# Performance work log

Hardware: AMD Instinct MI355X
Metric: run time of the kernel (lower is better)

The kernel has to match this reference:

```python
import math
import jax, jax.numpy as jnp
import numpy as np

B, S, HIDDEN = 1, 4096, 2048
HEADS, KVH = 16, 4
HD = HIDDEN // HEADS            # 128
GROUPS = HEADS // KVH           # 4
CHUNK = 1024                    # ring_attention_chunk_size
BASE = 500000.0
MAXPOS = 131072
ORIG = 8192
BFAST, BSLOW, MSCALE_CFG = 32.0, 1.0, 1.0
SCALING = MAXPOS / ORIG


def _yarn_inv_freq():
    dim = HD
    pos_freqs = BASE ** (np.arange(0, dim, 2, dtype=np.float32) / dim)
    extrap = 1.0 / pos_freqs
    interp = 1.0 / (SCALING * pos_freqs)
    low = max(math.floor(dim * math.log(ORIG / (BFAST * 2 * math.pi)) / (2 * math.log(BASE))), 0)
    high = min(math.ceil(dim * math.log(ORIG / (BSLOW * 2 * math.pi)) / (2 * math.log(BASE))), dim - 1)
    i = np.arange(dim // 2, dtype=np.float32)
    smooth = np.clip((i - low) / max(high - low, 1), 0.0, 1.0)  # i<low -> interp, i>high -> extrap
    inv = (1.0 - smooth) * interp + smooth * extrap
    return jnp.asarray(inv, jnp.float32)

INV_FREQ = _yarn_inv_freq()
MSCALE = (0.1 * math.log(SCALING) + 1.0) * MSCALE_CFG  # scaling > 1


def rotate_half(x):
    x1, x2 = jnp.split(x, 2, axis=-1)
    return jnp.concatenate((-x2, x1), axis=-1)


def ring_attention(q, k, v, chunk, causal=True):
    # q,k,v: [B,H,S,D]; kv_len divisible by chunk
    b, h, s, d = q.shape
    kv_len = k.shape[2]
    nc = kv_len // chunk
    scale = d ** (-0.5)
    k_chunks = jnp.moveaxis(k.reshape(b, h, nc, chunk, d), 2, 0)  # [nc,B,H,chunk,D]
    v_chunks = jnp.moveaxis(v.reshape(b, h, nc, chunk, d), 2, 0)
    kv_starts = jnp.arange(nc) * chunk
    q_idx = jnp.arange(s)[:, None]
    k_off = jnp.arange(chunk)[None, :]
    neg_inf = jnp.float32(-jnp.inf)

    def step(carry, inp):
        out, mx, se = carry
        kch, vch, kv_start = inp
        scores = jnp.einsum('bhqd,bhkd->bhqk', q, kch) * scale
        if causal:
            mask = (kv_start + k_off) > q_idx  # [S, chunk]
            scores = jnp.where(mask[None, None], neg_inf, scores)
        chunk_max = scores.max(axis=-1, keepdims=True)
        new_max = jnp.maximum(mx, chunk_max)
        exp_old = se * jnp.exp(mx - new_max)
        exp_chunk = jnp.exp(scores - new_max)
        exp_sum_chunk = exp_chunk.sum(axis=-1, keepdims=True)
        denom = exp_old + exp_sum_chunk + 1e-10
        out = out * (se / denom) + jnp.einsum('bhqk,bhkd->bhqd', exp_chunk, vch) / denom
        return (out, new_max, exp_old + exp_sum_chunk), None

    init = (jnp.zeros_like(q),
            jnp.full((b, h, s, 1), -jnp.inf, dtype=q.dtype),
            jnp.zeros((b, h, s, 1), dtype=q.dtype))
    (out, _, _), _ = jax.lax.scan(step, init, (k_chunks, v_chunks, kv_starts))
    return out


def setup_inputs() -> dict:
    key = jax.random.key(0)
    ks = jax.random.split(key, 5)
    hidden_states = jax.random.normal(ks[0], (B, S, HIDDEN), dtype=jnp.float32)
    position_ids = jnp.broadcast_to(jnp.arange(S, dtype=jnp.int32)[None, :], (B, S))
    sd = 1.0 / math.sqrt(HIDDEN)
    Wq = jax.random.normal(ks[1], (HIDDEN, HEADS * HD), dtype=jnp.float32) * sd
    Wk = jax.random.normal(ks[2], (HIDDEN, KVH * HD), dtype=jnp.float32) * sd
    Wv = jax.random.normal(ks[3], (HIDDEN, KVH * HD), dtype=jnp.float32) * sd
    Wo = jax.random.normal(ks[4], (HEADS * HD, HIDDEN), dtype=jnp.float32) * sd
    return {'hidden_states': hidden_states, 'position_ids': position_ids,
            'Wq': Wq, 'Wk': Wk, 'Wv': Wv, 'Wo': Wo}


def reference(hidden_states, position_ids, Wq, Wk, Wv, Wo):
    b, s, _ = hidden_states.shape
    q = (hidden_states @ Wq).reshape(b, s, HEADS, HD).transpose(0, 2, 1, 3)
    k = (hidden_states @ Wk).reshape(b, s, KVH, HD).transpose(0, 2, 1, 3)
    v = (hidden_states @ Wv).reshape(b, s, KVH, HD).transpose(0, 2, 1, 3)
    # YaRN rope
    freqs = position_ids.astype(jnp.float32)[:, :, None] * INV_FREQ[None, None, :]  # [B,S,HD/2]
    emb = jnp.concatenate((freqs, freqs), axis=-1)  # [B,S,HD]
    cos = (jnp.cos(emb) * MSCALE)[:, None]  # [B,1,S,HD]
    sin = (jnp.sin(emb) * MSCALE)[:, None]
    q = q * cos + rotate_half(q) * sin
    k = k * cos + rotate_half(k) * sin
    # GQA expand
    k = jnp.repeat(k, GROUPS, axis=1)
    v = jnp.repeat(v, GROUPS, axis=1)
    # ring path: use_ring_attention and kv_len > chunk
    attn = ring_attention(q, k, v, CHUNK, causal=True)
    attn = attn.transpose(0, 2, 1, 3).reshape(b, s, HEADS * HD)
    return attn @ Wo
```

## Files before the change

### kernel.cpp

```cpp
#include <hip/hip_runtime.h>
#include <cstdint>
#include <cstddef>


typedef unsigned short u16;
typedef unsigned int u32;
typedef float f32x4 __attribute__((ext_vector_type(4)));
typedef __bf16 bf16x8 __attribute__((ext_vector_type(8)));

__device__ __forceinline__ u16 f2bf(float f) {
    union { float f; u32 u; } v; v.f = f;
    u32 u = v.u;
    u += 0x7fffu + ((u >> 16) & 1u);
    return (u16)(u >> 16);
}
__device__ __forceinline__ float bf2f(u16 b) {
    union { u32 u; float f; } v; v.u = ((u32)b) << 16;
    return v.f;
}
__device__ __forceinline__ u16 f2h(float f) {
    union { _Float16 h; u16 u; } v; v.h = (_Float16)f; return v.u;
}
__device__ __forceinline__ float h2f(u16 u) {
    union { u16 u; _Float16 h; } v; v.u = u; return (float)v.h;
}

__device__ __forceinline__ void load16_to_lds(const void* g, void* l) {
    __builtin_amdgcn_global_load_lds((const __attribute__((address_space(1))) u32*)g,
                                     (__attribute__((address_space(3))) u32*)l,
                                     16, 0, 0);
}

#define MFMA16(a, b, c) __builtin_amdgcn_mfma_f32_16x16x32_bf16((a), (b), (c), 0, 0, 0)

__global__ __launch_bounds__(256) void convert_f32_bf16(const float* __restrict__ X,
                                                        u16* __restrict__ Y) {
    const int i = (blockIdx.x * 256 + threadIdx.x) * 4;
    const float4 v = *(const float4*)(X + i);
    union { u16 s[4]; uint2 u; } pk;
    pk.s[0] = f2bf(v.x); pk.s[1] = f2bf(v.y); pk.s[2] = f2bf(v.z); pk.s[3] = f2bf(v.w);
    *(uint2*)(Y + i) = pk.u;
}

__global__ __launch_bounds__(256) void transpose_w(const float* __restrict__ W,
                                                   u16* __restrict__ Wt, int N) {
    __shared__ float tile[64][65];
    const int n0 = blockIdx.x * 64, k0 = blockIdx.y * 64;
    const int tc = threadIdx.x & 63, tr = threadIdx.x >> 6;
#pragma unroll
    for (int i = 0; i < 64; i += 4)
        tile[tc][tr + i] = W[(size_t)(k0 + tr + i) * N + n0 + tc];
    __syncthreads();
#pragma unroll
    for (int i = 0; i < 64; i += 4)
        Wt[(size_t)(n0 + tr + i) * 2048 + k0 + tc] = f2bf(tile[tr + i][tc]);
}

__device__ __forceinline__ void store_out(float* p, float v) { *p = v; }
__device__ __forceinline__ void store_out(u16* p, float v) { *p = f2bf(v); }

template <typename OutT>
__global__ __launch_bounds__(256) void gemm_bt(const u16* __restrict__ A,
                                               const u16* __restrict__ Bt,
                                               OutT* __restrict__ C,
                                               int M, int N, int K) {
    __shared__ __align__(16) u16 sA[8192];
    __shared__ __align__(16) u16 sB[8192];
    const int t = threadIdx.x;
    const int lane = t & 63, w = t >> 6;
    const int quad = lane >> 4, l15 = lane & 15;
    const int m0 = blockIdx.x << 7, n0 = blockIdx.y << 7;
    const int wr4 = (w >> 1) * 4, wc4 = (w & 1) * 4;
    f32x4 acc[4][4] = {};
    for (int k0 = 0; k0 < K; k0 += 32) {
        __syncthreads();
#pragma unroll
        for (int r = 0; r < 2; ++r) {
            const int f = w * 2 + r;
            load16_to_lds(A + (size_t)(m0 + f * 16 + l15) * K + k0 + quad * 8, sA + f * 512);
            load16_to_lds(Bt + (size_t)(n0 + f * 16 + l15) * K + k0 + quad * 8, sB + f * 512);
        }
        __syncthreads();
        bf16x8 af[4], bb[4];
#pragma unroll
        for (int i = 0; i < 4; ++i)
            af[i] = *(const bf16x8*)(sA + (wr4 + i) * 512 + lane * 8);
#pragma unroll
        for (int j = 0; j < 4; ++j)
            bb[j] = *(const bf16x8*)(sB + (wc4 + j) * 512 + lane * 8);
#pragma unroll
        for (int i = 0; i < 4; ++i)
#pragma unroll
            for (int j = 0; j < 4; ++j)
                acc[i][j] = MFMA16(af[i], bb[j], acc[i][j]);
    }
#pragma unroll
    for (int i = 0; i < 4; ++i)
#pragma unroll
        for (int j = 0; j < 4; ++j) {
            const int row = m0 + (w >> 1) * 64 + i * 16 + quad * 4;
            const int col = n0 + (w & 1) * 64 + j * 16 + l15;
#pragma unroll
            for (int r = 0; r < 4; ++r)
                store_out(C + (size_t)(row + r) * N + col, acc[i][j][r]);
        }
}

__global__ __launch_bounds__(256) void rope_kernel(u16* __restrict__ Q,
                                                   u16* __restrict__ KV,
                                                   const int* __restrict__ pos_ids) {
    const int idx = blockIdx.x * 256 + threadIdx.x;
    const int NQ = 4096 * 16 * 64;
    u16* p;
    int s, i;
    if (idx < NQ) {
        s = idx >> 10;
        const int hi = idx & 1023;
        const int h = hi >> 6;
        i = hi & 63;
        p = Q + (size_t)s * 2048 + h * 128 + i;
    } else {
        const int k = idx - NQ;
        if (k >= 4096 * 4 * 64) return;
        s = k >> 8;
        const int hi = k & 255;
        const int h = hi >> 6;
        i = hi & 63;
        p = KV + (size_t)s * 1024 + h * 128 + i;
    }
    const float pf = (float)pos_ids[s];
    const float fi = (float)i;
    const float pos_freq = powf(500000.0f, fi * (1.0f / 64.0f));
    const float inv_ex = 1.0f / pos_freq;
    const float inv_in = inv_ex * (1.0f / 16.0f);
    const float sm = fminf(fmaxf((fi - 18.0f) * (1.0f / 17.0f), 0.0f), 1.0f);
    const float inv = (1.0f - sm) * inv_in + sm * inv_ex;
    const float ph = pf * inv;
    const float MS = 1.2772588722239781f;
    const float cs = cosf(ph) * MS, sn = sinf(ph) * MS;
    const float x1 = bf2f(p[0]), x2 = bf2f(p[64]);
    p[0] = f2bf(x1 * cs - x2 * sn);
    p[64] = f2bf(x2 * cs + x1 * sn);
}

__global__ __launch_bounds__(256) void transpose_v(const u16* __restrict__ KV,
                                                   u16* __restrict__ Vt) {
    __shared__ u16 tile[64 * 72];
    const int t = threadIdx.x;
    const int k0 = blockIdx.x * 64, d0 = blockIdx.y * 64, kvh = blockIdx.z;
#pragma unroll
    for (int k = 0; k < 4; ++k) {
        const int u = t + k * 256;
        const int key = u >> 4, dg = u & 15;
        const uint2 v = *(const uint2*)(KV + (size_t)(k0 + key) * 1024 + 512 + kvh * 128 + d0 + dg * 4);
        *(uint2*)(tile + key * 72 + dg * 4) = v;
    }
    __syncthreads();
#pragma unroll
    for (int k = 0; k < 4; ++k) {
        const int u = t + k * 256;
        const int d = u >> 4, kg = u & 15;
        union { u16 s[4]; uint2 v; } pk;
#pragma unroll
        for (int i = 0; i < 4; ++i) pk.s[i] = tile[(kg * 4 + i) * 72 + d];
        *(uint2*)(Vt + (size_t)(kvh * 128 + d0 + d) * 4096 + k0 + kg * 4) = pk.v;
    }
}

__global__ __launch_bounds__(256, 4) void attn_partial(const u16* __restrict__ Q,
                                                       const u16* __restrict__ KV,
                                                       const u16* __restrict__ Vt,
                                                       u16* __restrict__ part,
                                                       float* __restrict__ ml) {
    __shared__ __align__(16) u16 sK[8192];
    __shared__ __align__(16) u16 sV[8192];
    __shared__ __align__(16) u16 sP[2048];

    const int t = threadIdx.x;
    const int lane = t & 63, w = t >> 6;
    const int quad = lane >> 4, l15 = lane & 15;
    const int bid = blockIdx.x;
    const int u = bid >> 4, h = bid & 15, kvh = h >> 2;

    int qb, c;
    if (u < 16)      { qb = 16 + u; c = 0; }
    else if (u < 48) { const int r = u - 16; qb = 32 + (r >> 1); c = r & 1; }
    else if (u < 96) { const int r = u - 48; const int q3 = r / 3; qb = 48 + q3; c = r - q3 * 3; }
    else             { const int r = u - 96; const int g2 = r & 3; const int k = 16 - (r >> 2);
                       qb = (g2 << 4) + k - 1; c = g2; }
    const int g = qb >> 4;
    const int q0 = qb << 6, kv0 = c << 10;
    const int jmax = (c == g) ? ((qb & 15) + 1) : 16;

    {
        const u16* gq = Q + (size_t)(q0 + w * 16 + l15) * 2048 + h * 128 + quad * 8;
#pragma unroll
        for (int kc = 0; kc < 4; ++kc)
            load16_to_lds(gq + kc * 32, sK + (w * 4 + kc) * 512);
    }
    __syncthreads();
    bf16x8 af[4];
#pragma unroll
    for (int kc = 0; kc < 4; ++kc)
        af[kc] = *(const bf16x8*)(sK + (w * 4 + kc) * 512 + lane * 8);

    float m_c = -1e30f, l_c = 0.0f;
    f32x4 o_c[8] = {};
    const float SCALE = 0.08838834764831845f;
    const int qrow = q0 + w * 16 + l15;

    for (int j = 0; j < jmax; ++j) {
        const int kt0 = kv0 + (j << 6);
        __syncthreads();
        {
            const u16* gk = KV + (size_t)(kt0 + w * 16 + l15) * 1024 + kvh * 128 + quad * 8;
#pragma unroll
            for (int r = 0; r < 4; ++r)
                load16_to_lds(gk + r * 32, sK + (w * 4 + r) * 512);
#pragma unroll
            for (int r = 0; r < 4; ++r) {
                const int dt = w * 2 + (r >> 1), ks = r & 1;
                load16_to_lds(Vt + (size_t)(kvh * 128 + dt * 16 + l15) * 4096 + kt0 + ks * 32 + quad * 8,
                              sV + (w * 4 + r) * 512);
            }
        }
        __syncthreads();

        f32x4 sacc[4] = {};
#pragma unroll
        for (int j4 = 0; j4 < 4; ++j4)
#pragma unroll
            for (int kc = 0; kc < 4; ++kc) {
                const bf16x8 kf = *(const bf16x8*)(sK + (j4 * 4 + kc) * 512 + lane * 8);
                sacc[j4] = MFMA16(kf, af[kc], sacc[j4]);
            }

        float sv[4][4];
        if (kt0 == q0) {
#pragma unroll
            for (int j4 = 0; j4 < 4; ++j4)
#pragma unroll
                for (int r = 0; r < 4; ++r) {
                    const int key = kt0 + j4 * 16 + quad * 4 + r;
                    sv[j4][r] = (key > qrow) ? -1e30f : sacc[j4][r] * SCALE;
                }
        } else {
#pragma unroll
            for (int j4 = 0; j4 < 4; ++j4)
#pragma unroll
                for (int r = 0; r < 4; ++r)
                    sv[j4][r] = sacc[j4][r] * SCALE;
        }

        float mx = -1e30f;
#pragma unroll
        for (int j4 = 0; j4 < 4; ++j4)
#pragma unroll
            for (int r = 0; r < 4; ++r) mx = fmaxf(mx, sv[j4][r]);
        mx = fmaxf(mx, __shfl_xor(mx, 16, 64));
        mx = fmaxf(mx, __shfl_xor(mx, 32, 64));
        const float mn = fmaxf(m_c, mx);
        const float alpha = __expf(m_c - mn);
        float ps = 0.0f;
#pragma unroll
        for (int j4 = 0; j4 < 4; ++j4)
#pragma unroll
            for (int r = 0; r < 4; ++r) {
                const float pe = __expf(sv[j4][r] - mn);
                sv[j4][r] = pe;
                ps += pe;
            }
        ps += __shfl_xor(ps, 16, 64);
        ps += __shfl_xor(ps, 32, 64);
        l_c = l_c * alpha + ps;
        m_c = mn;
#pragma unroll
        for (int dt = 0; dt < 8; ++dt) o_c[dt] *= alpha;

#pragma unroll
        for (int ks = 0; ks < 2; ++ks) {
#pragma unroll
            for (int jj = 0; jj < 2; ++jj) {
                const int j4 = ks * 2 + jj;
#pragma unroll
                for (int p = 0; p < 2; ++p) {
                    const int k_in = jj * 16 + quad * 4 + p * 2;
                    const u32 pk = ((u32)f2bf(sv[j4][p * 2 + 1]) << 16) | f2bf(sv[j4][p * 2]);
                    *(u32*)(sP + w * 512 + ((k_in >> 3) * 16 + l15) * 8 + (k_in & 7)) = pk;
                }
            }
            const bf16x8 pf = *(const bf16x8*)(sP + w * 512 + lane * 8);
#pragma unroll
            for (int dt = 0; dt < 8; ++dt) {
                const bf16x8 vf = *(const bf16x8*)(sV + (dt * 2 + ks) * 512 + lane * 8);
                o_c[dt] = MFMA16(vf, pf, o_c[dt]);
            }
        }
    }

    const float invl = 1.0f / l_c;
#pragma unroll
    for (int dt = 0; dt < 8; ++dt)
#pragma unroll
        for (int r = 0; r < 4; ++r)
            part[(size_t)bid * 8192 + (dt * 16 + quad * 4 + r) * 64 + w * 16 + l15] =
                f2h(o_c[dt][r] * invl);
    if (quad == 0) {
        ml[(size_t)bid * 128 + (w * 16 + l15) * 2] = m_c;
        ml[(size_t)bid * 128 + (w * 16 + l15) * 2 + 1] = l_c;
    }
}

__global__ __launch_bounds__(256) void attn_merge(const u16* __restrict__ part,
                                                  const float* __restrict__ ml,
                                                  u16* __restrict__ attn) {
    const int b = blockIdx.x;
    const int qb = b >> 4, h = b & 15;
    const int g = qb >> 4, k15 = qb & 15;
    const int t = threadIdx.x;
    const int qrow = t & 63, dg = t >> 6;

    float o[32];
#pragma unroll
    for (int i = 0; i < 32; ++i) o[i] = 0.0f;
    float m_g = -1e30f, l_g = 0.0f;

    for (int c = 0; c <= g; ++c) {
        int u;
        if (c == g)      u = 96 + (15 - k15) * 4 + g;
        else if (g == 1) u = qb - 16;
        else if (g == 2) u = 16 + (qb - 32) * 2 + c;
        else             u = 48 + (qb - 48) * 3 + c;
        const int tile = u * 16 + h;
        const float m_c = ml[(size_t)tile * 128 + qrow * 2];
        const float l_c = ml[(size_t)tile * 128 + qrow * 2 + 1];
        const float mn = fmaxf(m_g, m_c);
        const float a = l_g * __expf(m_g - mn);
        const float eC = __expf(m_c - mn);
        const float sE = l_c * eC;
        const float d = a + sE + 1e-10f;
        const float f_old = l_g / d;
        const float f_new = sE / d;
#pragma unroll
        for (int i = 0; i < 32; ++i) {
            const float v = h2f(part[(size_t)tile * 8192 + (dg * 32 + i) * 64 + qrow]);
            o[i] = o[i] * f_old + v * f_new;
        }
        l_g = a + sE;
        m_g = mn;
    }

    u16* dst = attn + (size_t)(qb * 64 + qrow) * 2048 + h * 128 + dg * 32;
#pragma unroll
    for (int kq = 0; kq < 4; ++kq) {
        union { u16 s[8]; uint4 v; } pk;
#pragma unroll
        for (int i = 0; i < 8; ++i) pk.s[i] = f2bf(o[kq * 8 + i]);
        *(uint4*)(dst + kq * 8) = pk.v;
    }
}

extern "C" void kernel_launch(void* const* d_in, const int* in_sizes, int n_in,
                              void* d_out, int out_size, void* d_ws, size_t ws_size,
                              hipStream_t stream) {
    const float* X  = (const float*)d_in[0];
    const int* pos  = (const int*)d_in[1];
    const float* Wq = (const float*)d_in[2];
    const float* Wk = (const float*)d_in[3];
    const float* Wv = (const float*)d_in[4];
    const float* Wo = (const float*)d_in[5];
    float* out = (float*)d_out;
    char* ws = (char*)d_ws;

    u16*   part = (u16*)(ws);
    u16*   Xbf  = (u16*)(ws);
    u16*   Wqt  = (u16*)(ws + 16777216);
    u16*   Wkvt = (u16*)(ws + 25165824);
    u16*   Qbf  = (u16*)(ws + 41943040);
    u16*   attn = (u16*)(ws + 41943040);
    u16*   KVbf = (u16*)(ws + 58720256);
    u16*   Vt   = (u16*)(ws + 67108864);
    float* ml   = (float*)(ws + 71303168);
    u16*   Wot  = (u16*)(ws + 72613888);

    convert_f32_bf16<<<8192, 256, 0, stream>>>(X, Xbf);
    transpose_w<<<dim3(32, 32), 256, 0, stream>>>(Wq, Wqt, 2048);
    transpose_w<<<dim3(8, 32), 256, 0, stream>>>(Wk, Wkvt, 512);
    transpose_w<<<dim3(8, 32), 256, 0, stream>>>(Wv, Wkvt + (size_t)512 * 2048, 512);
    transpose_w<<<dim3(32, 32), 256, 0, stream>>>(Wo, Wot, 2048);

    gemm_bt<u16><<<dim3(32, 16), 256, 0, stream>>>(Xbf, Wqt, Qbf, 4096, 2048, 2048);
    gemm_bt<u16><<<dim3(32, 8), 256, 0, stream>>>(Xbf, Wkvt, KVbf, 4096, 1024, 2048);

    rope_kernel<<<20480, 256, 0, stream>>>(Qbf, KVbf, pos);
    transpose_v<<<dim3(64, 2, 4), 256, 0, stream>>>(KVbf, Vt);

    attn_partial<<<2560, 256, 0, stream>>>(Qbf, KVbf, Vt, part, ml);
    attn_merge<<<1024, 256, 0, stream>>>(part, ml, attn);

    gemm_bt<float><<<dim3(32, 16), 256, 0, stream>>>(attn, Wot, out, 4096, 2048, 2048);
}
```

Before: 501.7 us.

## Fuse Q/KV projections into one GEMM and use 128-row query tiles in attention

Q, K and V now come from a single GEMM writing an interleaved QKV buffer with row stride 3072, so one launch replaces two. The attention kernel now processes 128 query rows per block, with each wave handling two 16-row groups, so every K/V tile loaded into LDS serves twice as many queries. This halves the K/V traffic and the block count. The work schedule, partial layout and merge kernel are remapped to match. In exchange, register and LDS use grow (the P buffer is four times larger and launch bounds drop to 3 blocks per SM), and there are fewer blocks to balance the causal work.

```diff
diff --git a/kernel.cpp b/kernel.cpp
--- a/kernel.cpp
+++ b/kernel.cpp
@@ -106,8 +106,7 @@
         }
 }
 
-__global__ __launch_bounds__(256) void rope_kernel(u16* __restrict__ Q,
-                                                   u16* __restrict__ KV,
+__global__ __launch_bounds__(256) void rope_kernel(u16* __restrict__ QKV,
                                                    const int* __restrict__ pos_ids) {
     const int idx = blockIdx.x * 256 + threadIdx.x;
     const int NQ = 4096 * 16 * 64;
@@ -118,7 +117,7 @@
         const int hi = idx & 1023;
         const int h = hi >> 6;
         i = hi & 63;
-        p = Q + (size_t)s * 2048 + h * 128 + i;
+        p = QKV + (size_t)s * 3072 + h * 128 + i;
     } else {
         const int k = idx - NQ;
         if (k >= 4096 * 4 * 64) return;
@@ -126,7 +125,7 @@
         const int hi = k & 255;
         const int h = hi >> 6;
         i = hi & 63;
-        p = KV + (size_t)s * 1024 + h * 128 + i;
+        p = QKV + (size_t)s * 3072 + 2048 + h * 128 + i;
     }
     const float pf = (float)pos_ids[s];
     const float fi = (float)i;
@@ -143,7 +142,7 @@
     p[64] = f2bf(x2 * cs + x1 * sn);
 }
 
-__global__ __launch_bounds__(256) void transpose_v(const u16* __restrict__ KV,
+__global__ __launch_bounds__(256) void transpose_v(const u16* __restrict__ QKV,
                                                    u16* __restrict__ Vt) {
     __shared__ u16 tile[64 * 72];
     const int t = threadIdx.x;
@@ -152,7 +151,7 @@
     for (int k = 0; k < 4; ++k) {
         const int u = t + k * 256;
         const int key = u >> 4, dg = u & 15;
-        const uint2 v = *(const uint2*)(KV + (size_t)(k0 + key) * 1024 + 512 + kvh * 128 + d0 + dg * 4);
+        const uint2 v = *(const uint2*)(QKV + (size_t)(k0 + key) * 3072 + 2560 + kvh * 128 + d0 + dg * 4);
         *(uint2*)(tile + key * 72 + dg * 4) = v;
     }
     __syncthreads();
@@ -167,14 +166,13 @@
     }
 }
 
-__global__ __launch_bounds__(256, 4) void attn_partial(const u16* __restrict__ Q,
-                                                       const u16* __restrict__ KV,
+__global__ __launch_bounds__(256, 3) void attn_partial(const u16* __restrict__ QKV,
                                                        const u16* __restrict__ Vt,
                                                        u16* __restrict__ part,
                                                        float* __restrict__ ml) {
     __shared__ __align__(16) u16 sK[8192];
     __shared__ __align__(16) u16 sV[8192];
-    __shared__ __align__(16) u16 sP[2048];
+    __shared__ __align__(16) u16 sP[8192];
 
     const int t = threadIdx.x;
     const int lane = t & 63, w = t >> 6;
@@ -183,131 +181,163 @@
     const int u = bid >> 4, h = bid & 15, kvh = h >> 2;
 
     int qb, c;
-    if (u < 16)      { qb = 16 + u; c = 0; }
-    else if (u < 48) { const int r = u - 16; qb = 32 + (r >> 1); c = r & 1; }
-    else if (u < 96) { const int r = u - 48; const int q3 = r / 3; qb = 48 + q3; c = r - q3 * 3; }
-    else             { const int r = u - 96; const int g2 = r & 3; const int k = 16 - (r >> 2);
-                       qb = (g2 << 4) + k - 1; c = g2; }
-    const int g = qb >> 4;
-    const int q0 = qb << 6, kv0 = c << 10;
-    const int jmax = (c == g) ? ((qb & 15) + 1) : 16;
+    if (u < 8)       { qb = 8 + u; c = 0; }
+    else if (u < 24) { const int r = u - 8;  qb = 16 + (r >> 1); c = r & 1; }
+    else if (u < 48) { const int r = u - 24; const int q3 = r / 3; qb = 24 + q3; c = r - q3 * 3; }
+    else             { const int r = u - 48; const int k = r >> 2; const int g0 = r & 3;
+                       qb = g0 * 8 + (7 - k); c = g0; }
+    const int g = qb >> 3;
+    const int q0 = qb << 7, kv0 = c << 10;
+    const int jmax = (c == g) ? (2 * (qb & 7) + 2) : 16;
 
     {
-        const u16* gq = Q + (size_t)(q0 + w * 16 + l15) * 2048 + h * 128 + quad * 8;
-#pragma unroll
-        for (int kc = 0; kc < 4; ++kc)
-            load16_to_lds(gq + kc * 32, sK + (w * 4 + kc) * 512);
+        u16* dst0 = (w < 2) ? (u16*)sK : (u16*)sV;
+        const int fbase = (w & 1) * 8;
+#pragma unroll
+        for (int idx = 0; idx < 8; ++idx) {
+            const int qg = idx >> 2, kc = idx & 3;
+            load16_to_lds(QKV + (size_t)(q0 + w * 32 + qg * 16 + l15) * 3072 + h * 128 + kc * 32 + quad * 8,
+                          dst0 + (fbase + idx) * 512);
+        }
     }
     __syncthreads();
-    bf16x8 af[4];
-#pragma unroll
-    for (int kc = 0; kc < 4; ++kc)
-        af[kc] = *(const bf16x8*)(sK + (w * 4 + kc) * 512 + lane * 8);
-
-    float m_c = -1e30f, l_c = 0.0f;
-    f32x4 o_c[8] = {};
+    bf16x8 af[2][4];
+    {
+        const u16* src0 = (w < 2) ? (const u16*)sK : (const u16*)sV;
+        const int fbase = (w & 1) * 8;
+#pragma unroll
+        for (int qg = 0; qg < 2; ++qg)
+#pragma unroll
+            for (int kc = 0; kc < 4; ++kc)
+                af[qg][kc] = *(const bf16x8*)(src0 + (fbase + qg * 4 + kc) * 512 + lane * 8);
+    }
+
+    float m_c[2] = {-1e30f, -1e30f}, l_c[2] = {0.0f, 0.0f};
+    f32x4 o_c[8][2] = {};
     const float SCALE = 0.08838834764831845f;
-    const int qrow = q0 + w * 16 + l15;
 
     for (int j = 0; j < jmax; ++j) {
         const int kt0 = kv0 + (j << 6);
         __syncthreads();
         {
-            const u16* gk = KV + (size_t)(kt0 + w * 16 + l15) * 1024 + kvh * 128 + quad * 8;
-#pragma unroll
-            for (int r = 0; r < 4; ++r)
-                load16_to_lds(gk + r * 32, sK + (w * 4 + r) * 512);
+            const u16* gk = QKV + (size_t)(kt0 + w * 16 + l15) * 3072 + 2048 + kvh * 128 + quad * 8;
+#pragma unroll
+            for (int kc = 0; kc < 4; ++kc)
+                load16_to_lds(gk + kc * 32, sK + (w * 4 + kc) * 512);
 #pragma unroll
             for (int r = 0; r < 4; ++r) {
                 const int dt = w * 2 + (r >> 1), ks = r & 1;
                 load16_to_lds(Vt + (size_t)(kvh * 128 + dt * 16 + l15) * 4096 + kt0 + ks * 32 + quad * 8,
-                              sV + (w * 4 + r) * 512);
+                              sV + (dt * 2 + ks) * 512);
             }
         }
         __syncthreads();
 
-        f32x4 sacc[4] = {};
+        f32x4 sacc[4][2] = {};
 #pragma unroll
         for (int j4 = 0; j4 < 4; ++j4)
 #pragma unroll
             for (int kc = 0; kc < 4; ++kc) {
                 const bf16x8 kf = *(const bf16x8*)(sK + (j4 * 4 + kc) * 512 + lane * 8);
-                sacc[j4] = MFMA16(kf, af[kc], sacc[j4]);
+                sacc[j4][0] = MFMA16(kf, af[0][kc], sacc[j4][0]);
+                sacc[j4][1] = MFMA16(kf, af[1][kc], sacc[j4][1]);
             }
 
-        float sv[4][4];
-        if (kt0 == q0) {
+        const bool diag = (c == g) && ((j >> 1) == (qb & 7));
+        if (diag) {
 #pragma unroll
             for (int j4 = 0; j4 < 4; ++j4)
 #pragma unroll
-                for (int r = 0; r < 4; ++r) {
-                    const int key = kt0 + j4 * 16 + quad * 4 + r;
-                    sv[j4][r] = (key > qrow) ? -1e30f : sacc[j4][r] * SCALE;
+                for (int qg = 0; qg < 2; ++qg) {
+                    const int qrow = q0 + w * 32 + qg * 16 + l15;
+#pragma unroll
+                    for (int r = 0; r < 4; ++r) {
+                        const int key = kt0 + j4 * 16 + quad * 4 + r;
+                        sacc[j4][qg][r] = (key > qrow) ? -1e30f : sacc[j4][qg][r] * SCALE;
+                    }
                 }
         } else {
 #pragma unroll
             for (int j4 = 0; j4 < 4; ++j4)
 #pragma unroll
-                for (int r = 0; r < 4; ++r)
-                    sv[j4][r] = sacc[j4][r] * SCALE;
-        }
-
-        float mx = -1e30f;
-#pragma unroll
-        for (int j4 = 0; j4 < 4; ++j4)
-#pragma unroll
-            for (int r = 0; r < 4; ++r) mx = fmaxf(mx, sv[j4][r]);
-        mx = fmaxf(mx, __shfl_xor(mx, 16, 64));
-        mx = fmaxf(mx, __shfl_xor(mx, 32, 64));
-        const float mn = fmaxf(m_c, mx);
-        const float alpha = __expf(m_c - mn);
-        float ps = 0.0f;
-#pragma unroll
-        for (int j4 = 0; j4 < 4; ++j4)
-#pragma unroll
-            for (int r = 0; r < 4; ++r) {
-                const float pe = __expf(sv[j4][r] - mn);
-                sv[j4][r] = pe;
-                ps += pe;
-            }
-        ps += __shfl_xor(ps, 16, 64);
-        ps += __shfl_xor(ps, 32, 64);
-        l_c = l_c * alpha + ps;
-        m_c = mn;
-#pragma unroll
-        for (int dt = 0; dt < 8; ++dt) o_c[dt] *= alpha;
-
-#pragma unroll
-        for (int ks = 0; ks < 2; ++ks) {
+                for (int qg = 0; qg < 2; ++qg)
+#pragma unroll
+                    for (int r = 0; r < 4; ++r)
+                        sacc[j4][qg][r] *= SCALE;
+        }
+
+#pragma unroll
+        for (int qg = 0; qg < 2; ++qg) {
+            float mx = -1e30f;
+#pragma unroll
+            for (int j4 = 0; j4 < 4; ++j4)
+#pragma unroll
+                for (int r = 0; r < 4; ++r) mx = fmaxf(mx, sacc[j4][qg][r]);
+            mx = fmaxf(mx, __shfl_xor(mx, 16, 64));
+            mx = fmaxf(mx, __shfl_xor(mx, 32, 64));
+            const float mn = fmaxf(m_c[qg], mx);
+            const float alpha = __expf(m_c[qg] - mn);
+            float ps = 0.0f;
+#pragma unroll
+            for (int j4 = 0; j4 < 4; ++j4)
+#pragma unroll
+                for (int r = 0; r < 4; ++r) {
+                    const float pe = __expf(sacc[j4][qg][r] - mn);
+                    sacc[j4][qg][r] = pe;
+                    ps += pe;
+                }
+            ps += __shfl_xor(ps, 16, 64);
+            ps += __shfl_xor(ps, 32, 64);
+            l_c[qg] = l_c[qg] * alpha + ps;
+            m_c[qg] = mn;
+#pragma unroll
+            for (int dt = 0; dt < 8; ++dt) o_c[dt][qg] *= alpha;
+        }
+
+#pragma unroll
+        for (int ks = 0; ks < 2; ++ks)
 #pragma unroll
             for (int jj = 0; jj < 2; ++jj) {
                 const int j4 = ks * 2 + jj;
-#pragma unroll
-                for (int p = 0; p < 2; ++p) {
-                    const int k_in = jj * 16 + quad * 4 + p * 2;
-                    const u32 pk = ((u32)f2bf(sv[j4][p * 2 + 1]) << 16) | f2bf(sv[j4][p * 2]);
-                    *(u32*)(sP + w * 512 + ((k_in >> 3) * 16 + l15) * 8 + (k_in & 7)) = pk;
-                }
+                const int quadp = jj * 2 + (quad >> 1);
+#pragma unroll
+                for (int qg = 0; qg < 2; ++qg)
+#pragma unroll
+                    for (int pr = 0; pr < 2; ++pr) {
+                        const int r = pr * 2;
+                        const int jje = (quad & 1) * 4 + r;
+                        const u32 pk = ((u32)f2bf(sacc[j4][qg][r + 1]) << 16) | f2bf(sacc[j4][qg][r]);
+                        *(u32*)(sP + w * 2048 + (qg * 2 + ks) * 512 + (quadp * 16 + l15) * 8 + jje) = pk;
+                    }
             }
-            const bf16x8 pf = *(const bf16x8*)(sP + w * 512 + lane * 8);
+
+#pragma unroll
+        for (int ks = 0; ks < 2; ++ks) {
+            const bf16x8 pf0 = *(const bf16x8*)(sP + w * 2048 + (0 * 2 + ks) * 512 + lane * 8);
+            const bf16x8 pf1 = *(const bf16x8*)(sP + w * 2048 + (1 * 2 + ks) * 512 + lane * 8);
 #pragma unroll
             for (int dt = 0; dt < 8; ++dt) {
                 const bf16x8 vf = *(const bf16x8*)(sV + (dt * 2 + ks) * 512 + lane * 8);
-                o_c[dt] = MFMA16(vf, pf, o_c[dt]);
+                o_c[dt][0] = MFMA16(vf, pf0, o_c[dt][0]);
+                o_c[dt][1] = MFMA16(vf, pf1, o_c[dt][1]);
             }
         }
     }
 
-    const float invl = 1.0f / l_c;
-#pragma unroll
-    for (int dt = 0; dt < 8; ++dt)
-#pragma unroll
-        for (int r = 0; r < 4; ++r)
-            part[(size_t)bid * 8192 + (dt * 16 + quad * 4 + r) * 64 + w * 16 + l15] =
-                f2h(o_c[dt][r] * invl);
-    if (quad == 0) {
-        ml[(size_t)bid * 128 + (w * 16 + l15) * 2] = m_c;
-        ml[(size_t)bid * 128 + (w * 16 + l15) * 2 + 1] = l_c;
+#pragma unroll
+    for (int qg = 0; qg < 2; ++qg) {
+        const float invl = 1.0f / l_c[qg];
+        const int q = w * 32 + qg * 16 + l15;
+#pragma unroll
+        for (int dt = 0; dt < 8; ++dt)
+#pragma unroll
+            for (int r = 0; r < 4; ++r)
+                part[(size_t)bid * 16384 + (dt * 16 + quad * 4 + r) * 128 + q] =
+                    f2h(o_c[dt][qg][r] * invl);
+        if (quad == 0) {
+            ml[(size_t)bid * 256 + q * 2] = m_c[qg];
+            ml[(size_t)bid * 256 + q * 2 + 1] = l_c[qg];
+        }
     }
 }
 
@@ -316,9 +346,10 @@
                                                   u16* __restrict__ attn) {
     const int b = blockIdx.x;
     const int qb = b >> 4, h = b & 15;
-    const int g = qb >> 4, k15 = qb & 15;
+    const int g = qb >> 3;
     const int t = threadIdx.x;
-    const int qrow = t & 63, dg = t >> 6;
+    const int qrow = t & 127;
+    const int d0 = blockIdx.y * 64 + (t >> 7) * 32;
 
     float o[32];
 #pragma unroll
@@ -327,13 +358,13 @@
 
     for (int c = 0; c <= g; ++c) {
         int u;
-        if (c == g)      u = 96 + (15 - k15) * 4 + g;
-        else if (g == 1) u = qb - 16;
-        else if (g == 2) u = 16 + (qb - 32) * 2 + c;
-        else             u = 48 + (qb - 48) * 3 + c;
+        if (c == g)      u = 48 + (7 - (qb & 7)) * 4 + g;
+        else if (g == 1) u = qb - 8;
+        else if (g == 2) u = 8 + (qb - 16) * 2 + c;
+        else             u = 24 + (qb - 24) * 3 + c;
         const int tile = u * 16 + h;
-        const float m_c = ml[(size_t)tile * 128 + qrow * 2];
-        const float l_c = ml[(size_t)tile * 128 + qrow * 2 + 1];
+        const float m_c = ml[(size_t)tile * 256 + qrow * 2];
+        const float l_c = ml[(size_t)tile * 256 + qrow * 2 + 1];
         const float mn = fmaxf(m_g, m_c);
         const float a = l_g * __expf(m_g - mn);
         const float eC = __expf(m_c - mn);
@@ -343,14 +374,14 @@
         const float f_new = sE / d;
 #pragma unroll
         for (int i = 0; i < 32; ++i) {
-            const float v = h2f(part[(size_t)tile * 8192 + (dg * 32 + i) * 64 + qrow]);
+            const float v = h2f(part[(size_t)tile * 16384 + (d0 + i) * 128 + qrow]);
             o[i] = o[i] * f_old + v * f_new;
         }
         l_g = a + sE;
         m_g = mn;
     }
 
-    u16* dst = attn + (size_t)(qb * 64 + qrow) * 2048 + h * 128 + dg * 32;
+    u16* dst = attn + (size_t)(qb * 128 + qrow) * 2048 + h * 128 + d0;
 #pragma unroll
     for (int kq = 0; kq < 4; ++kq) {
         union { u16 s[8]; uint4 v; } pk;
@@ -374,29 +405,26 @@
 
     u16*   part = (u16*)(ws);
     u16*   Xbf  = (u16*)(ws);
-    u16*   Wqt  = (u16*)(ws + 16777216);
-    u16*   Wkvt = (u16*)(ws + 25165824);
-    u16*   Qbf  = (u16*)(ws + 41943040);
+    u16*   Wt   = (u16*)(ws + 16777216);
+    u16*   QKV  = (u16*)(ws + 41943040);
     u16*   attn = (u16*)(ws + 41943040);
-    u16*   KVbf = (u16*)(ws + 58720256);
     u16*   Vt   = (u16*)(ws + 67108864);
     float* ml   = (float*)(ws + 71303168);
     u16*   Wot  = (u16*)(ws + 72613888);
 
     convert_f32_bf16<<<8192, 256, 0, stream>>>(X, Xbf);
-    transpose_w<<<dim3(32, 32), 256, 0, stream>>>(Wq, Wqt, 2048);
-    transpose_w<<<dim3(8, 32), 256, 0, stream>>>(Wk, Wkvt, 512);
-    transpose_w<<<dim3(8, 32), 256, 0, stream>>>(Wv, Wkvt + (size_t)512 * 2048, 512);
+    transpose_w<<<dim3(32, 32), 256, 0, stream>>>(Wq, Wt, 2048);
+    transpose_w<<<dim3(8, 32), 256, 0, stream>>>(Wk, Wt + (size_t)2048 * 2048, 512);
+    transpose_w<<<dim3(8, 32), 256, 0, stream>>>(Wv, Wt + (size_t)2560 * 2048, 512);
     transpose_w<<<dim3(32, 32), 256, 0, stream>>>(Wo, Wot, 2048);
 
-    gemm_bt<u16><<<dim3(32, 16), 256, 0, stream>>>(Xbf, Wqt, Qbf, 4096, 2048, 2048);
-    gemm_bt<u16><<<dim3(32, 8), 256, 0, stream>>>(Xbf, Wkvt, KVbf, 4096, 1024, 2048);
-
-    rope_kernel<<<20480, 256, 0, stream>>>(Qbf, KVbf, pos);
-    transpose_v<<<dim3(64, 2, 4), 256, 0, stream>>>(KVbf, Vt);
-
-    attn_partial<<<2560, 256, 0, stream>>>(Qbf, KVbf, Vt, part, ml);
-    attn_merge<<<1024, 256, 0, stream>>>(part, ml, attn);
+    gemm_bt<u16><<<dim3(32, 24), 256, 0, stream>>>(Xbf, Wt, QKV, 4096, 3072, 2048);
+
+    rope_kernel<<<20480, 256, 0, stream>>>(QKV, pos);
+    transpose_v<<<dim3(64, 2, 4), 256, 0, stream>>>(QKV, Vt);
+
+    attn_partial<<<1280, 256, 0, stream>>>(QKV, Vt, part, ml);
+    attn_merge<<<dim3(512, 2), 256, 0, stream>>>(part, ml, attn);
 
     gemm_bt<float><<<dim3(32, 16), 256, 0, stream>>>(attn, Wot, out, 4096, 2048, 2048);
 }
```

Measured after the change: 504.9 us. No clear change (+0.6%).
